# Performance work log

Measured on AMD Instinct MI355X. Metric: run time of the kernel, lower is better.

Reference implementation:

```python
import jax, jax.numpy as jnp
import numpy as np

NUM_HEADS = 8
HIDDEN = 256


def _coattention(qf, rf, Wq, bq, Wk, bk, Wv, bv, Wo, bo, rel_emb):
    # qf, rf: (b, c, h, w); attention is axial over the height axis per width column.
    b, c, h, w = qf.shape
    T = rel_emb.shape[0]  # 2*max(h,w)-1
    q_in = qf.reshape(b, c, h * w).transpose(0, 2, 1)  # b (hw) c
    r_in = rf.reshape(b, c, h * w).transpose(0, 2, 1)
    q = (q_in @ Wq + bq).reshape(b, h, w, NUM_HEADS, HIDDEN).transpose(0, 3, 1, 2, 4)  # b n h w c
    k = (r_in @ Wk + bk).reshape(b, h, w, NUM_HEADS, HIDDEN).transpose(0, 3, 1, 2, 4)
    v = (r_in @ Wv + bv).reshape(b, h, w, NUM_HEADS, HIDDEN).transpose(0, 3, 1, 2, 4)
    scores = jnp.einsum('bnhwc,bnkwc->bnhwk', q, k)
    # relative index table: idx[i, j] = j - i, wrapped like torch negative indexing
    idx_h = (jnp.arange(h)[None, :] - jnp.arange(h)[:, None]) % T  # (h, h)
    idx_w = (jnp.arange(w)[None, :] - jnp.arange(w)[:, None]) % T  # (w, w); h == w required
    rel_h = rel_emb[idx_h]  # (h, h, c)
    rel_w = rel_emb[idx_w]  # (w, w, c)
    scores = scores + jnp.einsum('bnhwc,hkc->bnhwk', q, rel_h)
    scores = scores + jnp.einsum('bnhwc,wkc->bnhwk', q, rel_w)
    probs = jax.nn.softmax(scores / np.float32(np.sqrt(HIDDEN)), axis=-1)
    att = jnp.einsum('bnhwk,bnkwc->bnhwc', probs, v)
    out = att.transpose(0, 2, 3, 1, 4).reshape(b, h * w, NUM_HEADS * HIDDEN)  # b (hw) (n c)
    out = out @ Wo + bo
    return out.transpose(0, 2, 1).reshape(b, c, h, w)


def setup_inputs() -> dict:
    key = jax.random.key(0)
    ks = jax.random.split(key, 8)
    B, C, H, W = 4, 2048, 32, 32
    s = np.float32(0.02)
    return {
        'left_features': jax.random.normal(ks[0], (B, C, H, W), jnp.float32),
        'right_features': jax.random.normal(ks[1], (B, C, H, W), jnp.float32),
        'Wq': jax.random.normal(ks[2], (C, C), jnp.float32) * s,
        'bq': jnp.zeros((C,), jnp.float32),
        'Wk': jax.random.normal(ks[3], (C, C), jnp.float32) * s,
        'bk': jnp.zeros((C,), jnp.float32),
        'Wv': jax.random.normal(ks[4], (C, C), jnp.float32) * s,
        'bv': jnp.zeros((C,), jnp.float32),
        'Wo': jax.random.normal(ks[5], (C, C), jnp.float32) * s,
        'bo': jnp.zeros((C,), jnp.float32),
        'rel_emb': jax.random.normal(ks[6], (2 * max(H, W) - 1, HIDDEN), jnp.float32),
    }


def reference(left_features, right_features, Wq, bq, Wk, bk, Wv, bv, Wo, bo, rel_emb):
    weighted_r = _coattention(left_features, right_features, Wq, bq, Wk, bk, Wv, bv, Wo, bo, rel_emb)
    weighted_l = _coattention(right_features, left_features, Wq, bq, Wk, bk, Wv, bv, Wo, bo, rel_emb)
    left_attended = jnp.concatenate([left_features, weighted_r], axis=1)
    right_attended = jnp.concatenate([right_features, weighted_l], axis=1)
    return (left_attended, right_attended)
```

## Files before the change

### kernel.cpp

```cpp
#include <hip/hip_runtime.h>
#include <hip/hip_bf16.h>

typedef __attribute__((ext_vector_type(8))) short bf16x8;
typedef __attribute__((ext_vector_type(4))) float f32x4;

#define MFMA16(a, b, c) __builtin_amdgcn_mfma_f32_16x16x32_bf16((a), (b), (c), 0, 0, 0)

typedef __attribute__((address_space(1))) const void gconst_t;
typedef __attribute__((address_space(3))) void lds_t;
__device__ __forceinline__ void gload16(const void* gp, void* lp) {
    __builtin_amdgcn_global_load_lds((gconst_t*)gp, (lds_t*)lp, 16, 0, 0);
}

#define BAR() asm volatile("s_barrier" ::: "memory")
#define VMCNT4() asm volatile("s_waitcnt vmcnt(4)" ::: "memory")
#define VMCNT0() asm volatile("s_waitcnt vmcnt(0)" ::: "memory")
#define PRIO1() __builtin_amdgcn_s_setprio(1)
#define PRIO0() __builtin_amdgcn_s_setprio(0)

__global__ void transpose_cast(const float* __restrict__ in, __hip_bfloat16* __restrict__ out,
                               int R, int Ccols, float* __restrict__ copy_out) {
    __shared__ float tile[32][33];
    int r0 = blockIdx.y * 32, c0 = blockIdx.x * 32;
    size_t zoff = (size_t)blockIdx.z * R * Ccols;
    const float* ib = in + zoff;
    __hip_bfloat16* ob = out + zoff;
    int tx = threadIdx.x, ty = threadIdx.y;
    if (copy_out) {
        float* cb = copy_out + (size_t)blockIdx.z * 4194304;
#pragma unroll
        for (int i = ty; i < 32; i += 8) {
            float v = ib[(size_t)(r0 + i) * Ccols + c0 + tx];
            tile[i][tx] = v;
            cb[(size_t)(r0 + i) * Ccols + c0 + tx] = v;
        }
    } else {
#pragma unroll
        for (int i = ty; i < 32; i += 8)
            tile[i][tx] = ib[(size_t)(r0 + i) * Ccols + c0 + tx];
    }
    __syncthreads();
#pragma unroll
    for (int i = ty; i < 32; i += 8)
        ob[(size_t)(c0 + i) * R + r0 + tx] = __float2bfloat16(tile[tx][i]);
}

__global__ void conv_rel(const float* __restrict__ rel, __hip_bfloat16* __restrict__ relb) {
    int i = blockIdx.x * 256 + threadIdx.x;
    if (i < 64 * 256) {
        int r = i >> 8;
        relb[i] = __float2bfloat16(r < 63 ? rel[i] : 0.f);
    }
}

struct GArgs {
    const __hip_bfloat16* A[6];
    const __hip_bfloat16* B[6];
    void* C[6];
    const float* bias[6];
};

template <int MODE>
__global__ __launch_bounds__(512, 2) void gemm8p(GArgs ga, int N, int K,
                                                 float* __restrict__ dout) {
    __shared__ __align__(16) char smem[131072];

    const int gx = gridDim.x, gy = gridDim.y;
    int lid = blockIdx.x + gx * (blockIdx.y + gy * blockIdx.z);
    const int nwg = gx * gy * gridDim.z;
    int swz = (lid & 7) * (nwg >> 3) + (lid >> 3);
    const int z = swz / (gx * gy);
    int rem = swz - z * (gx * gy);
    const int by = rem / gx;
    const int bx = rem - by * gx;

    const __hip_bfloat16* __restrict__ A = ga.A[z];
    const __hip_bfloat16* __restrict__ B = ga.B[z];
    const float* __restrict__ bias = ga.bias[z];
    const int row0 = by * 256, col0 = bx * 256;

    const int tid = threadIdx.x;
    const int wave = tid >> 6, lane = tid & 63;
    const int l15 = lane & 15, lg = lane >> 4;
    const int wm = wave >> 2, wn = wave & 3;

    const int srow = tid >> 3;
    const int sch = (tid & 7) ^ (srow & 7);
    const int xr = (l15 & 7) << 4;
    const int off0 = (lg * 16) ^ xr;
    const int off1 = (64 + lg * 16) ^ xr;
    const int arow = wm * 16384;
    const int brow = 32768 + (wn >> 1) * 16384;
    const int bloc = (wn & 1) * 64;

    f32x4 acc[8][4] = {};
    bf16x8 a[4][2], bl[2][2], bh[2][2];

    const int NT = K >> 6;
    const int NI = NT >> 1;

    auto STAGE = [&](const __hip_bfloat16* base, int rowb, int T, int bufc, int isB, int h) {
#pragma unroll
        for (int L = 0; L < 2; ++L) {
            const __hip_bfloat16* g =
                base + (size_t)(rowb + h * 128 + L * 64 + srow) * K + T * 64 + sch * 8;
            gload16(g, smem + bufc * 65536 + isB * 32768 + h * 16384 + L * 8192 + wave * 1024);
        }
    };
    auto LDA = [&](int bufc, int mf, int ks) {
        return *(const bf16x8*)(smem + bufc * 65536 + arow + (mf * 16 + l15) * 128 +
                                (ks ? off1 : off0));
    };
    auto LDB = [&](int bufc, int nf, int ks) {
        return *(const bf16x8*)(smem + bufc * 65536 + brow + (bloc + nf * 16 + l15) * 128 +
                                (ks ? off1 : off0));
    };

#define READ_A(BUF, MOFF)                       \
    _Pragma("unroll") for (int mf = 0; mf < 4; ++mf) { \
        a[mf][0] = LDA(BUF, (MOFF) + mf, 0);    \
        a[mf][1] = LDA(BUF, (MOFF) + mf, 1);    \
    }
#define READ_B(BUF, NOFF, DST)                  \
    _Pragma("unroll") for (int nf = 0; nf < 2; ++nf) { \
        DST[nf][0] = LDB(BUF, (NOFF) + nf, 0);  \
        DST[nf][1] = LDB(BUF, (NOFF) + nf, 1);  \
    }
#define MFMA_QUAD(MOFF, NOFF, BR)                                                        \
    _Pragma("unroll") for (int mf = 0; mf < 4; ++mf)                                     \
    _Pragma("unroll") for (int nf = 0; nf < 2; ++nf) {                                   \
        acc[(MOFF) + mf][(NOFF) + nf] =                                                  \
            MFMA16(a[mf][0], BR[nf][0], acc[(MOFF) + mf][(NOFF) + nf]);                  \
        acc[(MOFF) + mf][(NOFF) + nf] =                                                  \
            MFMA16(a[mf][1], BR[nf][1], acc[(MOFF) + mf][(NOFF) + nf]);                  \
    }

    STAGE(B, col0, 0, 0, 1, 0);
    STAGE(A, row0, 0, 0, 0, 0);
    STAGE(A, row0, 0, 0, 0, 1);
    STAGE(B, col0, 0, 0, 1, 1);
    STAGE(B, col0, 1, 1, 1, 0);
    STAGE(A, row0, 1, 1, 0, 0);
    VMCNT4();
    BAR();

#pragma unroll 1
    for (int i = 0; i < NI; ++i) {
        const int t = 2 * i;
        const int T2 = (t + 2 < NT) ? t + 2 : t;
        const int T3 = (t + 3 < NT) ? t + 3 : t + 1;
        READ_A(0, 0); READ_B(0, 0, bl);
        STAGE(A, row0, t + 1, 1, 0, 1);
        BAR(); PRIO1(); MFMA_QUAD(0, 0, bl); PRIO0();

        READ_B(0, 2, bh);
        STAGE(B, col0, t + 1, 1, 1, 1);
        BAR(); PRIO1(); MFMA_QUAD(0, 2, bh); PRIO0();

        READ_A(0, 4);
        STAGE(B, col0, T2, 0, 1, 0);
        BAR(); PRIO1(); MFMA_QUAD(4, 2, bh); PRIO0();

        STAGE(A, row0, T2, 0, 0, 0);
        VMCNT4();
        BAR(); PRIO1(); MFMA_QUAD(4, 0, bl); PRIO0();

        READ_A(1, 0); READ_B(1, 0, bl);
        STAGE(A, row0, T2, 0, 0, 1);
        BAR(); PRIO1(); MFMA_QUAD(0, 0, bl); PRIO0();

        READ_B(1, 2, bh);
        STAGE(B, col0, T2, 0, 1, 1);
        BAR(); PRIO1(); MFMA_QUAD(0, 2, bh); PRIO0();

        READ_A(1, 4);
        STAGE(B, col0, T3, 1, 1, 0);
        BAR(); PRIO1(); MFMA_QUAD(4, 2, bh); PRIO0();

        STAGE(A, row0, T3, 1, 0, 0);
        VMCNT4();
        BAR(); PRIO1(); MFMA_QUAD(4, 0, bl); PRIO0();
    }
    VMCNT0();

    if (MODE == 0) {
        __hip_bfloat16* __restrict__ C = (__hip_bfloat16*)ga.C[z];
#pragma unroll
        for (int mf = 0; mf < 8; ++mf) {
            int m = row0 + wm * 128 + mf * 16 + lg * 4;
#pragma unroll
            for (int nf = 0; nf < 4; ++nf) {
                int n = col0 + wn * 64 + nf * 16 + l15;
                float bv = bias[n];
#pragma unroll
                for (int r = 0; r < 4; ++r)
                    C[(size_t)(m + r) * N + n] = __float2bfloat16(acc[mf][nf][r] + bv);
            }
        }
    } else {
        float* __restrict__ OB = dout + (size_t)z * 16777216;
#pragma unroll
        for (int mf = 0; mf < 8; ++mf) {
            int n0 = row0 + wm * 128 + mf * 16 + lg * 4;
#pragma unroll
            for (int nf = 0; nf < 4; ++nf) {
                int m = col0 + wn * 64 + nf * 16 + l15;
                size_t base = (size_t)(m >> 10) * 4194304 + (size_t)(m & 1023);
#pragma unroll
                for (int r = 0; r < 4; ++r) {
                    int n = n0 + r;
                    OB[base + (size_t)(2048 + n) * 1024] = acc[mf][nf][r] + bias[n];
                }
            }
        }
    }
#undef READ_A
#undef READ_B
#undef MFMA_QUAD
}

__global__ __launch_bounds__(256, 2) void attn_kernel(
    const __hip_bfloat16* __restrict__ Qa, const __hip_bfloat16* __restrict__ Ka,
    const __hip_bfloat16* __restrict__ Va, const __hip_bfloat16* __restrict__ Qb,
    const __hip_bfloat16* __restrict__ Kb, const __hip_bfloat16* __restrict__ Vb,
    const __hip_bfloat16* __restrict__ relb, __hip_bfloat16* __restrict__ Oa,
    __hip_bfloat16* __restrict__ Ob) {
    const int w = blockIdx.x;
    const int nh = blockIdx.y;
    const int zb = blockIdx.z;
    const int dir = zb >> 2, b = zb & 3;
    const __hip_bfloat16* __restrict__ Q = dir ? Qb : Qa;
    const __hip_bfloat16* __restrict__ K = dir ? Kb : Ka;
    const __hip_bfloat16* __restrict__ V = dir ? Vb : Va;
    __hip_bfloat16* __restrict__ O = dir ? Ob : Oa;

    __shared__ __align__(16) __hip_bfloat16 vt[256 * 40];
    __shared__ float ssc[32 * 32];
    __shared__ float es[32 * 64];
    __shared__ __align__(16) __hip_bfloat16 ps[32 * 32];

    const int tid = threadIdx.x;
    const int lane = tid & 63, wave = tid >> 6;
    const int l15 = lane & 15, lg = lane >> 4;
    const int mt = wave >> 1, nt = wave & 1;

    const size_t rowbase = ((size_t)b * 1024 + w) * 2048 + (size_t)nh * 256;

    for (int i = 0; i < 32; ++i) {
        int e = i * 256 + tid;
        int hk = e >> 8, c = e & 255;
        vt[c * 40 + hk] = V[rowbase + (size_t)hk * 65536 + c];
    }

    f32x4 sacc = {}, e0 = {}, e1 = {};
#pragma unroll
    for (int k8 = 0; k8 < 256; k8 += 32) {
        bf16x8 af = *(const bf16x8*)&Q[rowbase + (size_t)(mt * 16 + l15) * 65536 + k8 + lg * 8];
        bf16x8 bf = *(const bf16x8*)&K[rowbase + (size_t)(nt * 16 + l15) * 65536 + k8 + lg * 8];
        bf16x8 r0 = *(const bf16x8*)&relb[(size_t)(nt * 32 + l15) * 256 + k8 + lg * 8];
        bf16x8 r1 = *(const bf16x8*)&relb[(size_t)(nt * 32 + 16 + l15) * 256 + k8 + lg * 8];
        sacc = MFMA16(af, bf, sacc);
        e0 = MFMA16(af, r0, e0);
        e1 = MFMA16(af, r1, e1);
    }
#pragma unroll
    for (int r = 0; r < 4; ++r) {
        int row = mt * 16 + lg * 4 + r;
        ssc[row * 32 + nt * 16 + l15] = sacc[r];
        es[row * 64 + nt * 32 + l15] = e0[r];
        es[row * 64 + nt * 32 + 16 + l15] = e1[r];
    }
    __syncthreads();

    {
        int h = tid >> 3, sub = tid & 7;
        float v4[4];
        float mx = -1e30f;
#pragma unroll
        for (int i = 0; i < 4; ++i) {
            int k = sub * 4 + i;
            int dh = k - h; if (dh < 0) dh += 63;
            int dw = k - w; if (dw < 0) dw += 63;
            float s = (ssc[h * 32 + k] + es[h * 64 + dh] + es[h * 64 + dw]) * 0.0625f;
            v4[i] = s;
            mx = fmaxf(mx, s);
        }
        mx = fmaxf(mx, __shfl_xor(mx, 1));
        mx = fmaxf(mx, __shfl_xor(mx, 2));
        mx = fmaxf(mx, __shfl_xor(mx, 4));
        float sum = 0.f;
#pragma unroll
        for (int i = 0; i < 4; ++i) {
            v4[i] = __expf(v4[i] - mx);
            sum += v4[i];
        }
        sum += __shfl_xor(sum, 1);
        sum += __shfl_xor(sum, 2);
        sum += __shfl_xor(sum, 4);
        float inv = 1.f / sum;
#pragma unroll
        for (int i = 0; i < 4; ++i) ps[h * 32 + sub * 4 + i] = __float2bfloat16(v4[i] * inv);
    }
    __syncthreads();

    bf16x8 paf = *(const bf16x8*)&ps[(mt * 16 + l15) * 32 + lg * 8];
#pragma unroll
    for (int j = 0; j < 8; ++j) {
        int ct = nt * 8 + j;
        bf16x8 bv = *(const bf16x8*)&vt[(size_t)(ct * 16 + l15) * 40 + lg * 8];
        f32x4 oacc = {};
        oacc = MFMA16(paf, bv, oacc);
#pragma unroll
        for (int r = 0; r < 4; ++r) {
            int hh = mt * 16 + lg * 4 + r;
            O[rowbase + (size_t)hh * 65536 + ct * 16 + l15] = __float2bfloat16(oacc[r]);
        }
    }
}

extern "C" void kernel_launch(void* const* d_in, const int* in_sizes, int n_in, void* d_out,
                              int out_size, void* d_ws, size_t ws_size, hipStream_t stream) {
    const float* Xl = (const float*)d_in[0];
    const float* Xr = (const float*)d_in[1];
    const float* Wq = (const float*)d_in[2];
    const float* bq = (const float*)d_in[3];
    const float* Wk = (const float*)d_in[4];
    const float* bk = (const float*)d_in[5];
    const float* Wv = (const float*)d_in[6];
    const float* bv = (const float*)d_in[7];
    const float* Wo = (const float*)d_in[8];
    const float* bo = (const float*)d_in[9];
    const float* rel = (const float*)d_in[10];
    float* out = (float*)d_out;

    char* ws = (char*)d_ws;
    size_t off = 0;
    auto nxt = [&](size_t bytes) {
        void* p = ws + off;
        off += bytes;
        return p;
    };
    __hip_bfloat16* Xbl = (__hip_bfloat16*)nxt(16777216);
    __hip_bfloat16* Xbr = (__hip_bfloat16*)nxt(16777216);
    __hip_bfloat16* Wtq = (__hip_bfloat16*)nxt(8388608);
    __hip_bfloat16* Wtk = (__hip_bfloat16*)nxt(8388608);
    __hip_bfloat16* Wtv = (__hip_bfloat16*)nxt(8388608);
    __hip_bfloat16* Wto = (__hip_bfloat16*)nxt(8388608);
    __hip_bfloat16* relb = (__hip_bfloat16*)nxt(32768);
    __hip_bfloat16* Ql = (__hip_bfloat16*)nxt(16777216);
    __hip_bfloat16* Kl = (__hip_bfloat16*)nxt(16777216);
    __hip_bfloat16* Vl = (__hip_bfloat16*)nxt(16777216);
    __hip_bfloat16* Qr = (__hip_bfloat16*)nxt(16777216);
    __hip_bfloat16* Kr = (__hip_bfloat16*)nxt(16777216);
    __hip_bfloat16* Vr = (__hip_bfloat16*)nxt(16777216);
    __hip_bfloat16* At0 = Xbl;
    __hip_bfloat16* At1 = Xbr;

    dim3 tb(32, 8);
    transpose_cast<<<dim3(32, 64, 4), tb, 0, stream>>>(Xl, Xbl, 2048, 1024, out);
    transpose_cast<<<dim3(32, 64, 4), tb, 0, stream>>>(Xr, Xbr, 2048, 1024, out + 16777216);
    transpose_cast<<<dim3(64, 64, 1), tb, 0, stream>>>(Wq, Wtq, 2048, 2048, nullptr);
    transpose_cast<<<dim3(64, 64, 1), tb, 0, stream>>>(Wk, Wtk, 2048, 2048, nullptr);
    transpose_cast<<<dim3(64, 64, 1), tb, 0, stream>>>(Wv, Wtv, 2048, 2048, nullptr);
    transpose_cast<<<dim3(64, 64, 1), tb, 0, stream>>>(Wo, Wto, 2048, 2048, nullptr);
    conv_rel<<<64, 256, 0, stream>>>(rel, relb);

    GArgs g1 = {};
    g1.A[0] = Xbl; g1.A[1] = Xbl; g1.A[2] = Xbl;
    g1.A[3] = Xbr; g1.A[4] = Xbr; g1.A[5] = Xbr;
    g1.B[0] = Wtq; g1.B[1] = Wtk; g1.B[2] = Wtv;
    g1.B[3] = Wtq; g1.B[4] = Wtk; g1.B[5] = Wtv;
    g1.C[0] = Ql; g1.C[1] = Kl; g1.C[2] = Vl;
    g1.C[3] = Qr; g1.C[4] = Kr; g1.C[5] = Vr;
    g1.bias[0] = bq; g1.bias[1] = bk; g1.bias[2] = bv;
    g1.bias[3] = bq; g1.bias[4] = bk; g1.bias[5] = bv;
    gemm8p<0><<<dim3(8, 16, 6), 512, 0, stream>>>(g1, 2048, 2048, nullptr);

    attn_kernel<<<dim3(32, 8, 8), 256, 0, stream>>>(Ql, Kr, Vr, Qr, Kl, Vl, relb, At0, At1);

    GArgs g2 = {};
    g2.A[0] = Wto; g2.A[1] = Wto;
    g2.B[0] = At0; g2.B[1] = At1;
    g2.bias[0] = bo; g2.bias[1] = bo;
    gemm8p<1><<<dim3(16, 8, 2), 512, 0, stream>>>(g2, 2048, 2048, out);
}
```

Baseline: 353.8 us.

## Prefetch GEMM LDS fragments one phase ahead and batch weight transposes

The GEMM main loop is restructured so each phase issues the LDS reads for the next MFMA quad before running the current one. Separate A-low/A-high and double-buffered B-low registers let shared-memory reads overlap matrix math, and sched_barrier keeps the compiler from reordering them. The four weight transpose-casts are merged into one launch with a z-indexed argument struct, and the X transpose is specialised with constant sizes. The prefetching raises register pressure, and reads issued right after a barrier depend on the staged data having landed.

After: 386.7 us. 1.09x slower.

```diff
diff --git a/kernel.cpp b/kernel.cpp
--- a/kernel.cpp
+++ b/kernel.cpp
@@ -14,35 +14,50 @@
 
 #define BAR() asm volatile("s_barrier" ::: "memory")
 #define VMCNT4() asm volatile("s_waitcnt vmcnt(4)" ::: "memory")
-#define VMCNT0() asm volatile("s_waitcnt vmcnt(0)" ::: "memory")
+#define DRAIN() asm volatile("s_waitcnt vmcnt(0) lgkmcnt(0)" ::: "memory")
 #define PRIO1() __builtin_amdgcn_s_setprio(1)
 #define PRIO0() __builtin_amdgcn_s_setprio(0)
-
-__global__ void transpose_cast(const float* __restrict__ in, __hip_bfloat16* __restrict__ out,
-                               int R, int Ccols, float* __restrict__ copy_out) {
+#define SCHED0() __builtin_amdgcn_sched_barrier(0)
+
+__global__ void transpose_x(const float* __restrict__ in, __hip_bfloat16* __restrict__ out,
+                            float* __restrict__ copy_out) {
     __shared__ float tile[32][33];
     int r0 = blockIdx.y * 32, c0 = blockIdx.x * 32;
-    size_t zoff = (size_t)blockIdx.z * R * Ccols;
+    size_t zoff = (size_t)blockIdx.z * 2048 * 1024;
     const float* ib = in + zoff;
     __hip_bfloat16* ob = out + zoff;
+    float* cb = copy_out + (size_t)blockIdx.z * 4194304;
     int tx = threadIdx.x, ty = threadIdx.y;
-    if (copy_out) {
-        float* cb = copy_out + (size_t)blockIdx.z * 4194304;
-#pragma unroll
-        for (int i = ty; i < 32; i += 8) {
-            float v = ib[(size_t)(r0 + i) * Ccols + c0 + tx];
-            tile[i][tx] = v;
-            cb[(size_t)(r0 + i) * Ccols + c0 + tx] = v;
-        }
-    } else {
-#pragma unroll
-        for (int i = ty; i < 32; i += 8)
-            tile[i][tx] = ib[(size_t)(r0 + i) * Ccols + c0 + tx];
+#pragma unroll
+    for (int i = ty; i < 32; i += 8) {
+        float v = ib[(size_t)(r0 + i) * 1024 + c0 + tx];
+        tile[i][tx] = v;
+        cb[(size_t)(r0 + i) * 1024 + c0 + tx] = v;
     }
     __syncthreads();
 #pragma unroll
     for (int i = ty; i < 32; i += 8)
-        ob[(size_t)(c0 + i) * R + r0 + tx] = __float2bfloat16(tile[tx][i]);
+        ob[(size_t)(c0 + i) * 2048 + r0 + tx] = __float2bfloat16(tile[tx][i]);
+}
+
+struct TArgs {
+    const float* src[4];
+    __hip_bfloat16* dst[4];
+};
+__global__ void transpose_w4(TArgs ta) {
+    __shared__ float tile[32][33];
+    const int z = blockIdx.z;
+    const float* __restrict__ ib = ta.src[z];
+    __hip_bfloat16* __restrict__ ob = ta.dst[z];
+    int r0 = blockIdx.y * 32, c0 = blockIdx.x * 32;
+    int tx = threadIdx.x, ty = threadIdx.y;
+#pragma unroll
+    for (int i = ty; i < 32; i += 8)
+        tile[i][tx] = ib[(size_t)(r0 + i) * 2048 + c0 + tx];
+    __syncthreads();
+#pragma unroll
+    for (int i = ty; i < 32; i += 8)
+        ob[(size_t)(c0 + i) * 2048 + r0 + tx] = __float2bfloat16(tile[tx][i]);
 }
 
 __global__ void conv_rel(const float* __restrict__ rel, __hip_bfloat16* __restrict__ relb) {
@@ -94,7 +109,7 @@
     const int bloc = (wn & 1) * 64;
 
     f32x4 acc[8][4] = {};
-    bf16x8 a[4][2], bl[2][2], bh[2][2];
+    bf16x8 alo[4][2], ahi[4][2], bhi[2][2], blo0[2][2], blo1[2][2];
 
     const int NT = K >> 6;
     const int NI = NT >> 1;
@@ -116,24 +131,37 @@
                                 (ks ? off1 : off0));
     };
 
-#define READ_A(BUF, MOFF)                       \
+#define READ_ALO(BUF)                                  \
     _Pragma("unroll") for (int mf = 0; mf < 4; ++mf) { \
-        a[mf][0] = LDA(BUF, (MOFF) + mf, 0);    \
-        a[mf][1] = LDA(BUF, (MOFF) + mf, 1);    \
-    }
-#define READ_B(BUF, NOFF, DST)                  \
+        alo[mf][0] = LDA(BUF, mf, 0);                  \
+        alo[mf][1] = LDA(BUF, mf, 1);                  \
+    }
+#define READ_AHI(BUF)                                  \
+    _Pragma("unroll") for (int mf = 0; mf < 4; ++mf) { \
+        ahi[mf][0] = LDA(BUF, 4 + mf, 0);              \
+        ahi[mf][1] = LDA(BUF, 4 + mf, 1);              \
+    }
+#define READ_BHI(BUF)                                  \
     _Pragma("unroll") for (int nf = 0; nf < 2; ++nf) { \
-        DST[nf][0] = LDB(BUF, (NOFF) + nf, 0);  \
-        DST[nf][1] = LDB(BUF, (NOFF) + nf, 1);  \
-    }
-#define MFMA_QUAD(MOFF, NOFF, BR)                                                        \
-    _Pragma("unroll") for (int mf = 0; mf < 4; ++mf)                                     \
-    _Pragma("unroll") for (int nf = 0; nf < 2; ++nf) {                                   \
-        acc[(MOFF) + mf][(NOFF) + nf] =                                                  \
-            MFMA16(a[mf][0], BR[nf][0], acc[(MOFF) + mf][(NOFF) + nf]);                  \
-        acc[(MOFF) + mf][(NOFF) + nf] =                                                  \
-            MFMA16(a[mf][1], BR[nf][1], acc[(MOFF) + mf][(NOFF) + nf]);                  \
-    }
+        bhi[nf][0] = LDB(BUF, 2 + nf, 0);              \
+        bhi[nf][1] = LDB(BUF, 2 + nf, 1);              \
+    }
+#define READ_BLO(BUF, DST)                             \
+    _Pragma("unroll") for (int nf = 0; nf < 2; ++nf) { \
+        DST[nf][0] = LDB(BUF, nf, 0);                  \
+        DST[nf][1] = LDB(BUF, nf, 1);                  \
+    }
+#define MQ(AR, MOFF, NOFF, BR)                                          \
+    SCHED0();                                                           \
+    PRIO1();                                                            \
+    _Pragma("unroll") for (int mf = 0; mf < 4; ++mf)                    \
+    _Pragma("unroll") for (int nf = 0; nf < 2; ++nf) {                  \
+        acc[(MOFF) + mf][(NOFF) + nf] =                                 \
+            MFMA16(AR[mf][0], BR[nf][0], acc[(MOFF) + mf][(NOFF) + nf]); \
+        acc[(MOFF) + mf][(NOFF) + nf] =                                 \
+            MFMA16(AR[mf][1], BR[nf][1], acc[(MOFF) + mf][(NOFF) + nf]); \
+    }                                                                   \
+    PRIO0();
 
     STAGE(B, col0, 0, 0, 1, 0);
     STAGE(A, row0, 0, 0, 0, 0);
@@ -143,45 +171,57 @@
     STAGE(A, row0, 1, 1, 0, 0);
     VMCNT4();
     BAR();
+    READ_ALO(0);
+    READ_BLO(0, blo0);
 
 #pragma unroll 1
     for (int i = 0; i < NI; ++i) {
         const int t = 2 * i;
         const int T2 = (t + 2 < NT) ? t + 2 : t;
         const int T3 = (t + 3 < NT) ? t + 3 : t + 1;
-        READ_A(0, 0); READ_B(0, 0, bl);
         STAGE(A, row0, t + 1, 1, 0, 1);
-        BAR(); PRIO1(); MFMA_QUAD(0, 0, bl); PRIO0();
-
-        READ_B(0, 2, bh);
+        BAR();
+        READ_BHI(0);
+        MQ(alo, 0, 0, blo0);
+
         STAGE(B, col0, t + 1, 1, 1, 1);
-        BAR(); PRIO1(); MFMA_QUAD(0, 2, bh); PRIO0();
-
-        READ_A(0, 4);
+        BAR();
+        READ_AHI(0);
+        MQ(alo, 0, 2, bhi);
+
         STAGE(B, col0, T2, 0, 1, 0);
-        BAR(); PRIO1(); MFMA_QUAD(4, 2, bh); PRIO0();
+        BAR();
+        MQ(ahi, 4, 2, bhi);
 
         STAGE(A, row0, T2, 0, 0, 0);
         VMCNT4();
-        BAR(); PRIO1(); MFMA_QUAD(4, 0, bl); PRIO0();
-
-        READ_A(1, 0); READ_B(1, 0, bl);
+        BAR();
+        READ_ALO(1);
+        READ_BLO(1, blo1);
+        MQ(ahi, 4, 0, blo0);
+
         STAGE(A, row0, T2, 0, 0, 1);
-        BAR(); PRIO1(); MFMA_QUAD(0, 0, bl); PRIO0();
-
-        READ_B(1, 2, bh);
+        BAR();
+        READ_BHI(1);
+        MQ(alo, 0, 0, blo1);
+
         STAGE(B, col0, T2, 0, 1, 1);
-        BAR(); PRIO1(); MFMA_QUAD(0, 2, bh); PRIO0();
-
-        READ_A(1, 4);
+        BAR();
+        READ_AHI(1);
+        MQ(alo, 0, 2, bhi);
+
         STAGE(B, col0, T3, 1, 1, 0);
-        BAR(); PRIO1(); MFMA_QUAD(4, 2, bh); PRIO0();
+        BAR();
+        MQ(ahi, 4, 2, bhi);
 
         STAGE(A, row0, T3, 1, 0, 0);
         VMCNT4();
-        BAR(); PRIO1(); MFMA_QUAD(4, 0, bl); PRIO0();
-    }
-    VMCNT0();
+        BAR();
+        READ_ALO(0);
+        READ_BLO(0, blo0);
+        MQ(ahi, 4, 0, blo1);
+    }
+    DRAIN();
 
     if (MODE == 0) {
         __hip_bfloat16* __restrict__ C = (__hip_bfloat16*)ga.C[z];
@@ -214,9 +254,11 @@
             }
         }
     }
-#undef READ_A
-#undef READ_B
-#undef MFMA_QUAD
+#undef READ_ALO
+#undef READ_AHI
+#undef READ_BHI
+#undef READ_BLO
+#undef MQ
 }
 
 __global__ __launch_bounds__(256, 2) void attn_kernel(
@@ -357,12 +399,12 @@
     __hip_bfloat16* At1 = Xbr;
 
     dim3 tb(32, 8);
-    transpose_cast<<<dim3(32, 64, 4), tb, 0, stream>>>(Xl, Xbl, 2048, 1024, out);
-    transpose_cast<<<dim3(32, 64, 4), tb, 0, stream>>>(Xr, Xbr, 2048, 1024, out + 16777216);
-    transpose_cast<<<dim3(64, 64, 1), tb, 0, stream>>>(Wq, Wtq, 2048, 2048, nullptr);
-    transpose_cast<<<dim3(64, 64, 1), tb, 0, stream>>>(Wk, Wtk, 2048, 2048, nullptr);
-    transpose_cast<<<dim3(64, 64, 1), tb, 0, stream>>>(Wv, Wtv, 2048, 2048, nullptr);
-    transpose_cast<<<dim3(64, 64, 1), tb, 0, stream>>>(Wo, Wto, 2048, 2048, nullptr);
+    transpose_x<<<dim3(32, 64, 4), tb, 0, stream>>>(Xl, Xbl, out);
+    transpose_x<<<dim3(32, 64, 4), tb, 0, stream>>>(Xr, Xbr, out + 16777216);
+    TArgs tw;
+    tw.src[0] = Wq; tw.src[1] = Wk; tw.src[2] = Wv; tw.src[3] = Wo;
+    tw.dst[0] = Wtq; tw.dst[1] = Wtk; tw.dst[2] = Wtv; tw.dst[3] = Wto;
+    transpose_w4<<<dim3(64, 64, 4), tb, 0, stream>>>(tw);
     conv_rel<<<64, 256, 0, stream>>>(rel, relb);
 
     GArgs g1 = {};
```
